# Optimization experiments

Measured on AMD Instinct MI355X. Metric: run time of the kernel, lower is better.

Reference implementation:

```python
import jax, jax.numpy as jnp
import numpy as np

N_CHAN = 64
N_PTS = 2048
D_IN = 256
D_OUT = 256
N_FRAMES = 32  # config.n_frames; no_frames = N_FRAMES - 1


def setup_inputs() -> dict:
    key = jax.random.key(0)
    k1, k2, k3, k4, k5 = jax.random.split(key, 5)
    x = jax.random.normal(k1, (N_CHAN, N_PTS, D_IN), dtype=jnp.float32)
    t = jax.random.uniform(k2, (1, N_CHAN, 1), dtype=jnp.float32)
    model_idx = jax.random.randint(k3, (N_CHAN,), 0, N_CHAN)
    # per-channel weights, SIREN-style uniform init scale
    bound = 1.0 / np.sqrt(D_IN)
    W = jax.random.uniform(k4, (N_CHAN, D_IN, D_OUT), minval=-bound, maxval=bound, dtype=jnp.float32)
    B = jax.random.uniform(k5, (N_FRAMES, D_OUT), minval=-bound, maxval=bound, dtype=jnp.float32)
    return {"x": x, "t": t, "model_idx": model_idx, "W": W, "B": B}


def reference(x, t, model_idx, W, B):
    no_frames = N_FRAMES - 1
    # bias index per channel from the time coordinate: (t[0,:,0] * no_frames).long()
    bias_idx = (t[0, :, 0] * no_frames).astype(jnp.int32)  # [C]
    Wg = W[model_idx]          # [C, D_IN, D_OUT] gathered per-channel weights
    bg = B[bias_idx]           # [C, D_OUT] gathered per-channel biases
    # batched per-channel linear: x [C, N, D_IN] @ Wg [C, D_IN, D_OUT]
    out = jnp.einsum('cni,cio->cno', x, Wg) + bg[:, None, :]
    return out
```

## Files before the change

### kernel.cpp

```cpp
#include <hip/hip_runtime.h>
#include <hip/hip_bf16.h>


#define M_PTS 2048
#define K_DIM 256
#define N_DIM 256
#define BT_STRIDE 264

typedef float floatx4 __attribute__((ext_vector_type(4)));
typedef __bf16 bf16x4 __attribute__((ext_vector_type(4)));
typedef __bf16 bf16x8 __attribute__((ext_vector_type(8)));

__device__ __forceinline__ __bf16 cvt_bf16(float f) {
  unsigned u = __builtin_bit_cast(unsigned, f);
  unsigned r = (u + 0x7FFFu + ((u >> 16) & 1u)) >> 16;
  return __builtin_bit_cast(__bf16, (unsigned short)r);
}

__global__ __launch_bounds__(256) void fused_k(
    const float* __restrict__ X, const float* __restrict__ T,
    const int* __restrict__ MI, const float* __restrict__ W,
    const float* __restrict__ Bb, float* __restrict__ Out) {
  __shared__ __bf16 As[128 * 32];
  __shared__ __bf16 Bt[128 * BT_STRIDE];

  const int bid = blockIdx.x;
  const int c   = bid >> 4;
  const int mg  = (bid >> 1) & 7;
  const int nt  = bid & 1;
  const int n0  = nt * 128;

  const float* __restrict__ Xc = X + (size_t)c * (M_PTS * K_DIM);
  const float* __restrict__ Wc = W + (size_t)MI[c] * (K_DIM * N_DIM);

  const int tid  = threadIdx.x;
  const int lane = tid & 63;
  const int w    = tid >> 6;
  const int wm   = w & 1;
  const int wn   = w >> 1;
  const int r    = lane & 15;
  const int kg   = lane >> 4;

  {
    const int n  = tid & 127;
    const int kq = tid >> 7;
    const float* __restrict__ src = Wc + (size_t)(kq * 128) * N_DIM + n0 + n;
    __bf16* __restrict__ dst = &Bt[n * BT_STRIDE + kq * 128];
#pragma unroll 4
    for (int u = 0; u < 32; ++u) {
      bf16x4 v;
      v.x = cvt_bf16(src[(size_t)(u * 4 + 0) * N_DIM]);
      v.y = cvt_bf16(src[(size_t)(u * 4 + 1) * N_DIM]);
      v.z = cvt_bf16(src[(size_t)(u * 4 + 2) * N_DIM]);
      v.w = cvt_bf16(src[(size_t)(u * 4 + 3) * N_DIM]);
      *(bf16x4*)&dst[u * 4] = v;
    }
  }

  const int sm  = tid >> 1;
  const int skh = (tid & 1) * 16;
  const float* __restrict__ xrow = Xc + skh;
  __bf16* __restrict__ adst = &As[sm * 32 + skh];

  int bidx = (int)(T[c] * 31.0f);
  bidx = bidx < 0 ? 0 : (bidx > 31 ? 31 : bidx);
  const float* __restrict__ brow = Bb + bidx * N_DIM + n0 + wn * 64;
  float bv[4];
#pragma unroll
  for (int j = 0; j < 4; ++j) bv[j] = brow[j * 16 + r];

  float* __restrict__ Oc = Out + (size_t)c * (M_PTS * N_DIM);

  for (int mt2 = 0; mt2 < 2; ++mt2) {
    const int m0 = mg * 256 + mt2 * 128;
    const float* __restrict__ xsrc = xrow + (size_t)(m0 + sm) * K_DIM;
    floatx4 acc[4][4] = {};

    for (int kt = 0; kt < 8; ++kt) {
      const int k0 = kt * 32;
      __syncthreads();
      {
        floatx4 f0 = *(const floatx4*)(xsrc + k0 + 0);
        floatx4 f1 = *(const floatx4*)(xsrc + k0 + 4);
        floatx4 f2 = *(const floatx4*)(xsrc + k0 + 8);
        floatx4 f3 = *(const floatx4*)(xsrc + k0 + 12);
        bf16x8 h0, h1;
#pragma unroll
        for (int v = 0; v < 4; ++v) {
          h0[v]     = cvt_bf16(f0[v]);
          h0[v + 4] = cvt_bf16(f1[v]);
          h1[v]     = cvt_bf16(f2[v]);
          h1[v + 4] = cvt_bf16(f3[v]);
        }
        *(bf16x8*)&adst[0] = h0;
        *(bf16x8*)&adst[8] = h1;
      }
      __syncthreads();

      bf16x8 a[4], b[4];
#pragma unroll
      for (int i = 0; i < 4; ++i)
        a[i] = *(const bf16x8*)&As[(wm * 64 + i * 16 + r) * 32 + kg * 8];
#pragma unroll
      for (int j = 0; j < 4; ++j)
        b[j] = *(const bf16x8*)&Bt[(wn * 64 + j * 16 + r) * BT_STRIDE + k0 + kg * 8];
#pragma unroll
      for (int i = 0; i < 4; ++i)
#pragma unroll
        for (int j = 0; j < 4; ++j)
          acc[i][j] = __builtin_amdgcn_mfma_f32_16x16x32_bf16(a[i], b[j], acc[i][j], 0, 0, 0);
    }

#pragma unroll
    for (int i = 0; i < 4; ++i) {
#pragma unroll
      for (int j = 0; j < 4; ++j) {
        const int col = n0 + wn * 64 + j * 16 + r;
#pragma unroll
        for (int v = 0; v < 4; ++v) {
          const int row = m0 + wm * 64 + i * 16 + kg * 4 + v;
          Oc[(size_t)row * N_DIM + col] = acc[i][j][v] + bv[j];
        }
      }
    }
  }
}

extern "C" void kernel_launch(void* const* d_in, const int* in_sizes, int n_in,
                              void* d_out, int out_size, void* d_ws, size_t ws_size,
                              hipStream_t stream) {
  const float* X   = (const float*)d_in[0];
  const float* T   = (const float*)d_in[1];
  const int* MI    = (const int*)d_in[2];
  const float* W   = (const float*)d_in[3];
  const float* Bb  = (const float*)d_in[4];
  float* Out       = (float*)d_out;

  fused_k<<<dim3(1024), dim3(256), 0, stream>>>(X, T, MI, W, Bb, Out);
}
```

Baseline: 271.4 us.

## Load X fragments directly from global into registers, drop A shared-memory staging

Each wave now reads its own A operand fragments of X straight from global memory and converts them to bf16 in registers. This removes the shared-memory A tile and the two block barriers per k-step. The bias is folded into the accumulator's initial value, and the k-loop is unrolled by two. In exchange, rows of X that were shared through LDS are now loaded separately by the two waves with the same wm, and each lane reads 32-byte strided chunks, which coalesces less well.

After: 291.3 us. 7.4% more time.

```diff
diff --git a/kernel.cpp b/kernel.cpp
--- a/kernel.cpp
+++ b/kernel.cpp
@@ -21,7 +21,6 @@
     const float* __restrict__ X, const float* __restrict__ T,
     const int* __restrict__ MI, const float* __restrict__ W,
     const float* __restrict__ Bb, float* __restrict__ Out) {
-  __shared__ __bf16 As[128 * 32];
   __shared__ __bf16 Bt[128 * BT_STRIDE];
 
   const int bid = blockIdx.x;
@@ -57,11 +56,6 @@
     }
   }
 
-  const int sm  = tid >> 1;
-  const int skh = (tid & 1) * 16;
-  const float* __restrict__ xrow = Xc + skh;
-  __bf16* __restrict__ adst = &As[sm * 32 + skh];
-
   int bidx = (int)(T[c] * 31.0f);
   bidx = bidx < 0 ? 0 : (bidx > 31 ? 31 : bidx);
   const float* __restrict__ brow = Bb + bidx * N_DIM + n0 + wn * 64;
@@ -69,38 +63,37 @@
 #pragma unroll
   for (int j = 0; j < 4; ++j) bv[j] = brow[j * 16 + r];
 
+  __syncthreads();
+
   float* __restrict__ Oc = Out + (size_t)c * (M_PTS * N_DIM);
 
   for (int mt2 = 0; mt2 < 2; ++mt2) {
     const int m0 = mg * 256 + mt2 * 128;
-    const float* __restrict__ xsrc = xrow + (size_t)(m0 + sm) * K_DIM;
-    floatx4 acc[4][4] = {};
+    const float* __restrict__ xbase =
+        Xc + (size_t)(m0 + wm * 64 + r) * K_DIM + kg * 8;
 
+    floatx4 acc[4][4];
+#pragma unroll
+    for (int i = 0; i < 4; ++i)
+#pragma unroll
+      for (int j = 0; j < 4; ++j)
+        acc[i][j] = (floatx4){bv[j], bv[j], bv[j], bv[j]};
+
+#pragma unroll 2
     for (int kt = 0; kt < 8; ++kt) {
       const int k0 = kt * 32;
-      __syncthreads();
-      {
-        floatx4 f0 = *(const floatx4*)(xsrc + k0 + 0);
-        floatx4 f1 = *(const floatx4*)(xsrc + k0 + 4);
-        floatx4 f2 = *(const floatx4*)(xsrc + k0 + 8);
-        floatx4 f3 = *(const floatx4*)(xsrc + k0 + 12);
-        bf16x8 h0, h1;
+      bf16x8 a[4], b[4];
+#pragma unroll
+      for (int i = 0; i < 4; ++i) {
+        const float* p = xbase + (size_t)i * 16 * K_DIM + k0;
+        floatx4 f0 = *(const floatx4*)(p);
+        floatx4 f1 = *(const floatx4*)(p + 4);
 #pragma unroll
         for (int v = 0; v < 4; ++v) {
-          h0[v]     = cvt_bf16(f0[v]);
-          h0[v + 4] = cvt_bf16(f1[v]);
-          h1[v]     = cvt_bf16(f2[v]);
-          h1[v + 4] = cvt_bf16(f3[v]);
+          a[i][v]     = cvt_bf16(f0[v]);
+          a[i][v + 4] = cvt_bf16(f1[v]);
         }
-        *(bf16x8*)&adst[0] = h0;
-        *(bf16x8*)&adst[8] = h1;
       }
-      __syncthreads();
-
-      bf16x8 a[4], b[4];
-#pragma unroll
-      for (int i = 0; i < 4; ++i)
-        a[i] = *(const bf16x8*)&As[(wm * 64 + i * 16 + r) * 32 + kg * 8];
 #pragma unroll
       for (int j = 0; j < 4; ++j)
         b[j] = *(const bf16x8*)&Bt[(wn * 64 + j * 16 + r) * BT_STRIDE + k0 + kg * 8];
@@ -119,7 +112,7 @@
 #pragma unroll
         for (int v = 0; v < 4; ++v) {
           const int row = m0 + wm * 64 + i * 16 + kg * 4 + v;
-          Oc[(size_t)row * N_DIM + col] = acc[i][j][v] + bv[j];
+          Oc[(size_t)row * N_DIM + col] = acc[i][j][v];
         }
       }
     }
```
